# Kernel optimization log

Measured on AMD Instinct MI355X. Metric: run time of the kernel, lower is better.

## Reference

```python
import jax, jax.numpy as jnp
import numpy as np

N = 100000      # nodes
E = 1600000     # edges
IN, H1, H2, OUT = 128, 128, 64, 128  # layer_channel = [128, (128+128)//2, (128+128)//4, 128]


def setup_inputs() -> dict:
    key = jax.random.key(0)
    ks = jax.random.split(key, 11)
    w = lambda k, s: (jax.random.normal(k, s, jnp.float32) * 0.05)
    return {
        "x": jax.random.normal(ks[0], (N, IN), jnp.float32),
        "edge_index": jax.random.randint(ks[1], (2, E), 0, N),
        "gcn1_w": w(ks[2], (IN, H1)),   "gcn1_b": jnp.zeros((H1,), jnp.float32),
        "fc2_w": w(ks[3], (H1, H1)),   # nn.Linear weight [out, in]
        "gcn3_w": w(ks[4], (H1, H2)),   "gcn3_b": jnp.zeros((H2,), jnp.float32),
        "fc4_w": w(ks[5], (H2, H2)),
        "gcn5_w": w(ks[6], (H2, OUT)),  "gcn5_b": jnp.zeros((OUT,), jnp.float32),
        "fc6_w": w(ks[7], (OUT, OUT)),
    }


def _gcn_norm(edge_index):
    # PyG GCNConv default: add self-loops, symmetric normalization D^-1/2 (A+I) D^-1/2
    loop = jnp.arange(N, dtype=edge_index.dtype)
    src = jnp.concatenate([edge_index[0], loop])
    dst = jnp.concatenate([edge_index[1], loop])
    deg = jax.ops.segment_sum(jnp.ones_like(src, jnp.float32), dst, num_segments=N)
    dinv = jnp.where(deg > 0, jax.lax.rsqrt(jnp.maximum(deg, 1.0)), 0.0)
    norm = dinv[src] * dinv[dst]  # [E+N]
    return src, dst, norm


def _gcn_conv(x, W, b, src, dst, norm):
    h = x @ W                              # [N, d_out]
    msg = h[src] * norm[:, None]           # gather + scale over edges
    return jax.ops.segment_sum(msg, dst, num_segments=N) + b


def reference(x, edge_index, gcn1_w, gcn1_b, fc2_w, gcn3_w, gcn3_b, fc4_w, gcn5_w, gcn5_b, fc6_w):
    src, dst, norm = _gcn_norm(edge_index)
    relu = jax.nn.relu
    z1 = relu(_gcn_conv(x, gcn1_w, gcn1_b, src, dst, norm))
    z1 = relu(z1 + z1 @ fc2_w.T)
    z2 = relu(_gcn_conv(z1, gcn3_w, gcn3_b, src, dst, norm))
    z2 = relu(z2 + z2 @ fc4_w.T)
    z3 = relu(_gcn_conv(z2, gcn5_w, gcn5_b, src, dst, norm))
    z3 = relu(z3 + z3 @ fc6_w.T)
    return z3
```

## Files before the change

kernel.cpp:

```cpp
#include <hip/hip_runtime.h>
#include <cstdint>
#include <cstddef>

#define NN 100000
#define NE 1600000
#define NBB 391

typedef short short8 __attribute__((ext_vector_type(8)));
typedef float floatx4 __attribute__((ext_vector_type(4)));
typedef uint32_t u32x4 __attribute__((ext_vector_type(4)));
typedef unsigned short u16;
typedef uint32_t u32;


static __global__ void k_zero(int* __restrict__ gh) {
    int i = threadIdx.x;
    if (i < NBB + 1) gh[i] = 0;
}

static __global__ __launch_bounds__(1024) void k_bhist(const int* __restrict__ dst,
                                                       int* __restrict__ gh) {
    __shared__ int h[NBB + 1];
    int t = threadIdx.x;
    for (int i = t; i < NBB; i += 1024) h[i] = 0;
    __syncthreads();
    int e0 = blockIdx.x * 4096;
#pragma unroll
    for (int j = 0; j < 4; j++) {
        int e = e0 + j * 1024 + t;
        if (e < NE) atomicAdd(&h[dst[e] >> 8], 1);
    }
    __syncthreads();
    for (int i = t; i < NBB; i += 1024)
        if (h[i]) atomicAdd(&gh[i], h[i]);
}

static __global__ void k_bscan(const int* __restrict__ gh, int* __restrict__ gbase,
                               int* __restrict__ gcur) {
    __shared__ int sd[512];
    int t = threadIdx.x;
    int v = (t < NBB) ? gh[t] : 0;
    sd[t] = v;
    __syncthreads();
    for (int off = 1; off < 512; off <<= 1) {
        int x = (t >= off) ? sd[t - off] : 0;
        __syncthreads();
        sd[t] += x;
        __syncthreads();
    }
    int excl = (t > 0) ? sd[t - 1] : 0;
    if (t < NBB) {
        gbase[t] = excl;
        gcur[t] = excl;
    }
    if (t == NBB) gbase[NBB] = excl;
}

static __global__ __launch_bounds__(1024) void k_bscatter(const int* __restrict__ src,
                                                          const int* __restrict__ dst,
                                                          int* __restrict__ gcur,
                                                          int2* __restrict__ staging) {
    __shared__ int h[NBB + 1];
    __shared__ int base[NBB + 1];
    int t = threadIdx.x;
    for (int i = t; i < NBB; i += 1024) h[i] = 0;
    __syncthreads();
    int e0 = blockIdx.x * 4096;
    int b[4], l[4], sv[4], dv[4];
#pragma unroll
    for (int j = 0; j < 4; j++) {
        int e = e0 + j * 1024 + t;
        b[j] = -1;
        if (e < NE) {
            sv[j] = src[e];
            dv[j] = dst[e];
            b[j] = dv[j] >> 8;
            l[j] = atomicAdd(&h[b[j]], 1);
        }
    }
    __syncthreads();
    for (int i = t; i < NBB; i += 1024)
        if (h[i]) base[i] = atomicAdd(&gcur[i], h[i]);
    __syncthreads();
#pragma unroll
    for (int j = 0; j < 4; j++)
        if (b[j] >= 0) staging[base[b[j]] + l[j]] = make_int2(sv[j], dv[j]);
}

static __global__ __launch_bounds__(1024) void k_blocal(const int2* __restrict__ staging,
                                                        const int* __restrict__ gbase,
                                                        int* __restrict__ deg,
                                                        float* __restrict__ dinv) {
    __shared__ int cnt[256];
    int b = blockIdx.x;
    int t = threadIdx.x;
    if (t < 256) cnt[t] = 0;
    __syncthreads();
    int end = gbase[b + 1];
    for (int i = gbase[b] + t; i < end; i += 1024)
        atomicAdd(&cnt[staging[i].y & 255], 1);
    __syncthreads();
    if (t < 256) {
        int node = (b << 8) + t;
        if (node < NN) {
            int d = cnt[t] + 1;
            deg[node] = d;
            dinv[node] = rsqrtf((float)d);
        }
    }
}

static __global__ void k_scan1(const int* __restrict__ deg, int* __restrict__ row_ptr,
                               int* __restrict__ bsums) {
    __shared__ int sd[256];
    int t = threadIdx.x;
    int base = blockIdx.x * 1024;
    int v[4];
    int s = 0;
#pragma unroll
    for (int j = 0; j < 4; j++) {
        int i = base + t * 4 + j;
        int c = (i < NN) ? (deg[i] - 1) : 0;
        v[j] = s;
        s += c;
    }
    sd[t] = s;
    __syncthreads();
    for (int off = 1; off < 256; off <<= 1) {
        int x = (t >= off) ? sd[t - off] : 0;
        __syncthreads();
        sd[t] += x;
        __syncthreads();
    }
    int excl = (t > 0) ? sd[t - 1] : 0;
#pragma unroll
    for (int j = 0; j < 4; j++) {
        int i = base + t * 4 + j;
        if (i < NN) row_ptr[i] = excl + v[j];
    }
    if (t == 255) bsums[blockIdx.x] = sd[255];
}

static __global__ void k_scan2(int* __restrict__ bsums, int nb) {
    __shared__ int sd[128];
    int t = threadIdx.x;
    int v = (t < nb) ? bsums[t] : 0;
    sd[t] = v;
    __syncthreads();
    for (int off = 1; off < 128; off <<= 1) {
        int x = (t >= off) ? sd[t - off] : 0;
        __syncthreads();
        sd[t] += x;
        __syncthreads();
    }
    if (t < nb) bsums[t] = sd[t] - v;
}

static __global__ void k_scan3(int* __restrict__ row_ptr, const int* __restrict__ bsums) {
    int i = blockIdx.x * 256 + threadIdx.x;
    if (i < NN) {
        row_ptr[i] += bsums[i >> 10];
    } else if (i == NN) {
        row_ptr[NN] = NE;
    }
}

static __global__ __launch_bounds__(1024) void k_bfill(const int2* __restrict__ staging,
                                                       const int* __restrict__ gbase,
                                                       const int* __restrict__ row_ptr,
                                                       int* __restrict__ csr_src) {
    __shared__ int cnt[256];
    int b = blockIdx.x;
    int t = threadIdx.x;
    if (t < 256) cnt[t] = 0;
    __syncthreads();
    int end = gbase[b + 1];
    for (int i = gbase[b] + t; i < end; i += 1024) {
        int2 ed = staging[i];
        int r = atomicAdd(&cnt[ed.y & 255], 1);
        csr_src[row_ptr[ed.y] + r] = ed.x;
    }
}

__device__ __forceinline__ void split_bf16(float f, short& hi, short& lo) {
    union { float f; uint32_t u; } x;
    x.f = f;
    uint32_t uh = x.u + 0x7FFFu + ((x.u >> 16) & 1u);
    hi = (short)(uh >> 16);
    union { uint32_t u; float f; } hf;
    hf.u = (uh >> 16) << 16;
    float r = f - hf.f;
    union { float f; uint32_t u; } y;
    y.f = r;
    uint32_t ul = y.u + 0x7FFFu + ((y.u >> 16) & 1u);
    lo = (short)(ul >> 16);
}

__device__ __forceinline__ u16 f2bf(float f) {
    union { float f; uint32_t u; } x;
    x.f = f;
    uint32_t r = x.u + 0x7FFFu + ((x.u >> 16) & 1u);
    return (u16)(r >> 16);
}

__device__ __forceinline__ float bf2f(u16 h) {
    union { uint32_t u; float f; } x;
    x.u = ((uint32_t)h) << 16;
    return x.f;
}

__device__ __forceinline__ u32 packsplit(float f) {
    short h, l;
    split_bf16(f, h, l);
    return (u32)(u16)h | ((u32)(u16)l << 16);
}

__device__ __forceinline__ float unpacksplit(u32 u) {
    return bf2f((u16)(u & 0xFFFFu)) + bf2f((u16)(u >> 16));
}

__device__ __forceinline__ void acc2(uint32_t u, float& a0, float& a1) {
    union { uint32_t u; float f; } lo, hi;
    lo.u = u << 16;
    hi.u = u & 0xFFFF0000u;
    a0 += lo.f;
    a1 += hi.f;
}

struct WDesc {
    const float* W;
    short* fh;
    short* fl;
    int din, dout, transb, base, total;
};
struct WPrepArgs { WDesc d[6]; };

static __global__ void k_wprep(WPrepArgs args) {
    int tid = blockIdx.x * 256 + threadIdx.x;
#pragma unroll
    for (int i = 0; i < 6; i++) {
        const WDesc& D = args.d[i];
        if (tid >= D.base && tid < D.base + D.total) {
            int local = tid - D.base;
            int lane = local & 63;
            int rest = local >> 6;
            int kst = D.din >> 5;
            int ks = rest % kst;
            int ntile = rest / kst;
            int n = ntile * 16 + (lane & 15);
            int k0 = ks * 32 + (lane >> 4) * 8;
#pragma unroll
            for (int j = 0; j < 8; j++) {
                int k = k0 + j;
                float v = D.transb ? D.W[(size_t)n * D.din + k]
                                   : D.W[(size_t)k * D.dout + n];
                short h, l;
                split_bf16(v, h, l);
                D.fh[(size_t)local * 8 + j] = h;
                D.fl[(size_t)local * 8 + j] = l;
            }
        }
    }
}

template <int DIN, int DOUT, int MT, int AMODE, int OMODE, bool RESID, bool BIAS, bool SCALE>
__global__ __launch_bounds__(256) void k_mgemm(const void* __restrict__ Av,
                                               const short* __restrict__ fh,
                                               const short* __restrict__ fl,
                                               const float* __restrict__ bias,
                                               const float* __restrict__ dinv,
                                               void* __restrict__ C) {
    static_assert(!RESID || DIN == DOUT, "residual needs square");
    constexpr int KST = DIN / 32;
    constexpr int NTW = DOUT / 64;
    const int t = threadIdx.x;
    const int wave = t >> 6;
    const int lane = t & 63;
    const int r16 = lane & 15;
    const int kq = lane >> 4;

    const float* Af = (const float*)Av;
    const u32*   Au = (const u32*)Av;

    short8 bh[NTW][KST], bl[NTW][KST];
#pragma unroll
    for (int nt = 0; nt < NTW; nt++) {
        int ntile = wave * NTW + nt;
#pragma unroll
        for (int ks = 0; ks < KST; ks++) {
            size_t o = ((size_t)(ntile * KST + ks) * 64 + lane) * 8;
            bh[nt][ks] = *(const short8*)(fh + o);
            bl[nt][ks] = *(const short8*)(fl + o);
        }
    }

    const int m0b = blockIdx.x * (MT * 16);
#pragma unroll 1
    for (int mt = 0; mt < MT; mt++) {
        const int m0 = m0b + mt * 16;
        if (m0 >= NN) break;
        const int ra = min(m0 + r16, NN - 1);

        floatx4 acc[NTW];
#pragma unroll
        for (int nt = 0; nt < NTW; nt++) acc[nt] = (floatx4){0.f, 0.f, 0.f, 0.f};

        if constexpr (AMODE == 1) {
            const float* Ap = Af + (size_t)ra * DIN + kq * 8;
#pragma unroll
            for (int ks = 0; ks < KST; ks++) {
                float4 f0 = *(const float4*)(Ap + ks * 32);
                float4 f1 = *(const float4*)(Ap + ks * 32 + 4);
                float fe[8] = {f0.x, f0.y, f0.z, f0.w, f1.x, f1.y, f1.z, f1.w};
                short8 ah;
#pragma unroll
                for (int j = 0; j < 8; j++) ah[j] = (short)f2bf(fe[j]);
#pragma unroll
                for (int nt = 0; nt < NTW; nt++) {
                    acc[nt] = __builtin_amdgcn_mfma_f32_16x16x32_bf16(ah, bh[nt][ks], acc[nt], 0, 0, 0);
                    acc[nt] = __builtin_amdgcn_mfma_f32_16x16x32_bf16(ah, bl[nt][ks], acc[nt], 0, 0, 0);
                }
            }
        } else {
            const u32* Ap = Au + (size_t)ra * DIN + kq * 8;
#pragma unroll
            for (int ks = 0; ks < KST; ks++) {
                u32x4 p0 = *(const u32x4*)(Ap + ks * 32);
                u32x4 p1 = *(const u32x4*)(Ap + ks * 32 + 4);
                short8 ah, al;
#pragma unroll
                for (int j = 0; j < 4; j++) {
                    ah[j] = (short)(p0[j] & 0xFFFFu);
                    al[j] = (short)(p0[j] >> 16);
                    ah[j + 4] = (short)(p1[j] & 0xFFFFu);
                    al[j + 4] = (short)(p1[j] >> 16);
                }
#pragma unroll
                for (int nt = 0; nt < NTW; nt++) {
                    acc[nt] = __builtin_amdgcn_mfma_f32_16x16x32_bf16(ah, bh[nt][ks], acc[nt], 0, 0, 0);
                    acc[nt] = __builtin_amdgcn_mfma_f32_16x16x32_bf16(ah, bl[nt][ks], acc[nt], 0, 0, 0);
                    acc[nt] = __builtin_amdgcn_mfma_f32_16x16x32_bf16(al, bh[nt][ks], acc[nt], 0, 0, 0);
                }
            }
        }

#pragma unroll
        for (int nt = 0; nt < NTW; nt++) {
            int col = (wave * NTW + nt) * 16 + r16;
#pragma unroll
            for (int r = 0; r < 4; r++) {
                int row = m0 + kq * 4 + r;
                if (row < NN) {
                    float v = acc[nt][r];
                    if constexpr (RESID)
                        v = fmaxf(v + unpacksplit(Au[(size_t)row * DIN + col]), 0.f);
                    if constexpr (BIAS) v = fmaxf(v + bias[col], 0.f);
                    if constexpr (SCALE) v *= dinv[row];
                    if constexpr (OMODE == 0)
                        ((float*)C)[(size_t)row * DOUT + col] = v;
                    else if constexpr (OMODE == 1)
                        ((u16*)C)[(size_t)row * DOUT + col] = f2bf(v);
                    else
                        ((u32*)C)[(size_t)row * DOUT + col] = packsplit(v);
                }
            }
        }
    }
}

template <int DIN, int DMID, int DOUT, int MT, bool RESID1, bool BIAS1,
          bool SCALE2, bool RESID2, int OMODE2>
__global__ __launch_bounds__(256) void k_mfused(const u32* __restrict__ A,
                                                const short* __restrict__ f1h,
                                                const short* __restrict__ f1l,
                                                const short* __restrict__ f2h,
                                                const short* __restrict__ f2l,
                                                const float* __restrict__ bias1,
                                                const float* __restrict__ dinv,
                                                void* __restrict__ C) {
    static_assert(!RESID1 || DIN == DMID, "resid1 needs square stage1");
    static_assert(!RESID2 || DMID == DOUT, "resid2 needs square stage2");
    constexpr int KST1 = DIN / 32;
    constexpr int NTW1 = DMID / 64;
    constexpr int KST2 = DMID / 32;
    constexpr int NTW2 = DOUT / 64;
    constexpr int LDW = DMID + 4;
    __shared__ u32 lds[16][LDW];

    const int t = threadIdx.x;
    const int wave = t >> 6;
    const int lane = t & 63;
    const int r16 = lane & 15;
    const int kq = lane >> 4;

    short8 b1h[NTW1][KST1], b1l[NTW1][KST1];
#pragma unroll
    for (int nt = 0; nt < NTW1; nt++) {
        int ntile = wave * NTW1 + nt;
#pragma unroll
        for (int ks = 0; ks < KST1; ks++) {
            size_t o = ((size_t)(ntile * KST1 + ks) * 64 + lane) * 8;
            b1h[nt][ks] = *(const short8*)(f1h + o);
            b1l[nt][ks] = *(const short8*)(f1l + o);
        }
    }
    short8 b2h[NTW2][KST2], b2l[NTW2][KST2];
#pragma unroll
    for (int nt = 0; nt < NTW2; nt++) {
        int ntile = wave * NTW2 + nt;
#pragma unroll
        for (int ks = 0; ks < KST2; ks++) {
            size_t o = ((size_t)(ntile * KST2 + ks) * 64 + lane) * 8;
            b2h[nt][ks] = *(const short8*)(f2h + o);
            b2l[nt][ks] = *(const short8*)(f2l + o);
        }
    }

    const int m0b = blockIdx.x * (MT * 16);
#pragma unroll 1
    for (int mt = 0; mt < MT; mt++) {
        const int m0 = m0b + mt * 16;
        if (m0 >= NN) break;
        const int ra = min(m0 + r16, NN - 1);

        floatx4 acc1[NTW1];
#pragma unroll
        for (int nt = 0; nt < NTW1; nt++) acc1[nt] = (floatx4){0.f, 0.f, 0.f, 0.f};
        {
            const u32* Ap = A + (size_t)ra * DIN + kq * 8;
#pragma unroll
            for (int ks = 0; ks < KST1; ks++) {
                u32x4 p0 = *(const u32x4*)(Ap + ks * 32);
                u32x4 p1 = *(const u32x4*)(Ap + ks * 32 + 4);
                short8 ah, al;
#pragma unroll
                for (int j = 0; j < 4; j++) {
                    ah[j] = (short)(p0[j] & 0xFFFFu);
                    al[j] = (short)(p0[j] >> 16);
                    ah[j + 4] = (short)(p1[j] & 0xFFFFu);
                    al[j + 4] = (short)(p1[j] >> 16);
                }
#pragma unroll
                for (int nt = 0; nt < NTW1; nt++) {
                    acc1[nt] = __builtin_amdgcn_mfma_f32_16x16x32_bf16(ah, b1h[nt][ks], acc1[nt], 0, 0, 0);
                    acc1[nt] = __builtin_amdgcn_mfma_f32_16x16x32_bf16(ah, b1l[nt][ks], acc1[nt], 0, 0, 0);
                    acc1[nt] = __builtin_amdgcn_mfma_f32_16x16x32_bf16(al, b1h[nt][ks], acc1[nt], 0, 0, 0);
                }
            }
        }
#pragma unroll
        for (int nt = 0; nt < NTW1; nt++) {
            int col = (wave * NTW1 + nt) * 16 + r16;
#pragma unroll
            for (int r = 0; r < 4; r++) {
                int row = m0 + kq * 4 + r;
                float v = acc1[nt][r];
                if constexpr (RESID1) {
                    if (row < NN) v = fmaxf(v + unpacksplit(A[(size_t)row * DIN + col]), 0.f);
                }
                if constexpr (BIAS1) v = fmaxf(v + bias1[col], 0.f);
                lds[kq * 4 + r][col] = packsplit(v);
            }
        }
        __syncthreads();

        floatx4 acc2[NTW2];
#pragma unroll
        for (int nt = 0; nt < NTW2; nt++) acc2[nt] = (floatx4){0.f, 0.f, 0.f, 0.f};
#pragma unroll
        for (int ks = 0; ks < KST2; ks++) {
            const u32* lp = &lds[r16][ks * 32 + kq * 8];
            u32x4 p0 = *(const u32x4*)lp;
            u32x4 p1 = *(const u32x4*)(lp + 4);
            short8 ah, al;
#pragma unroll
            for (int j = 0; j < 4; j++) {
                ah[j] = (short)(p0[j] & 0xFFFFu);
                al[j] = (short)(p0[j] >> 16);
                ah[j + 4] = (short)(p1[j] & 0xFFFFu);
                al[j + 4] = (short)(p1[j] >> 16);
            }
#pragma unroll
            for (int nt = 0; nt < NTW2; nt++) {
                acc2[nt] = __builtin_amdgcn_mfma_f32_16x16x32_bf16(ah, b2h[nt][ks], acc2[nt], 0, 0, 0);
                acc2[nt] = __builtin_amdgcn_mfma_f32_16x16x32_bf16(ah, b2l[nt][ks], acc2[nt], 0, 0, 0);
                acc2[nt] = __builtin_amdgcn_mfma_f32_16x16x32_bf16(al, b2h[nt][ks], acc2[nt], 0, 0, 0);
            }
        }

#pragma unroll
        for (int nt = 0; nt < NTW2; nt++) {
            int col = (wave * NTW2 + nt) * 16 + r16;
#pragma unroll
            for (int r = 0; r < 4; r++) {
                int row = m0 + kq * 4 + r;
                if (row < NN) {
                    float v = acc2[nt][r];
                    if constexpr (RESID2)
                        v = fmaxf(v + unpacksplit(lds[kq * 4 + r][col]), 0.f);
                    if constexpr (SCALE2) v *= dinv[row];
                    if constexpr (OMODE2 == 0)
                        ((float*)C)[(size_t)row * DOUT + col] = v;
                    else if constexpr (OMODE2 == 1)
                        ((u16*)C)[(size_t)row * DOUT + col] = f2bf(v);
                    else
                        ((u32*)C)[(size_t)row * DOUT + col] = packsplit(v);
                }
            }
        }
        __syncthreads();
    }
}

template <int D, bool BIAS_RELU>
__global__ __launch_bounds__(256) void k_agg(const u16* __restrict__ hs,
                                             const float* __restrict__ dinv,
                                             const int* __restrict__ row_ptr,
                                             const int* __restrict__ csr_src,
                                             const float* __restrict__ bias,
                                             u32* __restrict__ out) {
    constexpr int V = D / 64;
    int node = blockIdx.x * 4 + (threadIdx.x >> 6);
    int lane = threadIdx.x & 63;
    if (node >= NN) return;
    const int off = lane * V;

    float a0 = 0.f, a1 = 0.f;
    if constexpr (V == 2) {
        uint32_t u = ((const uint32_t*)(hs + (size_t)node * D))[lane];
        acc2(u, a0, a1);
    } else {
        a0 = bf2f(hs[(size_t)node * D + lane]);
    }

    int e = row_ptr[node];
    const int end = row_ptr[node + 1];

    for (; e + 8 <= end; e += 8) {
        int s[8];
#pragma unroll
        for (int i = 0; i < 8; i++) s[i] = csr_src[e + i];
        if constexpr (V == 2) {
            uint32_t v[8];
#pragma unroll
            for (int i = 0; i < 8; i++) v[i] = ((const uint32_t*)(hs + (size_t)s[i] * D))[lane];
#pragma unroll
            for (int i = 0; i < 8; i++) acc2(v[i], a0, a1);
        } else {
            u16 v[8];
#pragma unroll
            for (int i = 0; i < 8; i++) v[i] = hs[(size_t)s[i] * D + lane];
#pragma unroll
            for (int i = 0; i < 8; i++) a0 += bf2f(v[i]);
        }
    }
    for (; e + 4 <= end; e += 4) {
        int s[4];
#pragma unroll
        for (int i = 0; i < 4; i++) s[i] = csr_src[e + i];
        if constexpr (V == 2) {
            uint32_t v[4];
#pragma unroll
            for (int i = 0; i < 4; i++) v[i] = ((const uint32_t*)(hs + (size_t)s[i] * D))[lane];
#pragma unroll
            for (int i = 0; i < 4; i++) acc2(v[i], a0, a1);
        } else {
            u16 v[4];
#pragma unroll
            for (int i = 0; i < 4; i++) v[i] = hs[(size_t)s[i] * D + lane];
#pragma unroll
            for (int i = 0; i < 4; i++) a0 += bf2f(v[i]);
        }
    }
    for (; e < end; e++) {
        int s = csr_src[e];
        if constexpr (V == 2) {
            uint32_t u = ((const uint32_t*)(hs + (size_t)s * D))[lane];
            acc2(u, a0, a1);
        } else {
            a0 += bf2f(hs[(size_t)s * D + lane]);
        }
    }

    const float di = dinv[node];
    a0 *= di;
    if constexpr (V == 2) a1 *= di;
    if constexpr (BIAS_RELU) {
        a0 = fmaxf(a0 + bias[off], 0.f);
        if constexpr (V == 2) a1 = fmaxf(a1 + bias[off + 1], 0.f);
    }
    u32* po = out + (size_t)node * D + off;
    if constexpr (V == 2) {
        uint2 w;
        w.x = packsplit(a0);
        w.y = packsplit(a1);
        *(uint2*)po = w;
    } else {
        *po = packsplit(a0);
    }
}


extern "C" void kernel_launch(void* const* d_in, const int* in_sizes, int n_in,
                              void* d_out, int out_size, void* d_ws, size_t ws_size,
                              hipStream_t stream) {
    const float* x   = (const float*)d_in[0];
    const int*   ei  = (const int*)d_in[1];
    const float* g1w = (const float*)d_in[2];
    const float* g1b = (const float*)d_in[3];
    const float* f2w = (const float*)d_in[4];
    const float* g3w = (const float*)d_in[5];
    const float* g3b = (const float*)d_in[6];
    const float* f4w = (const float*)d_in[7];
    const float* g5w = (const float*)d_in[8];
    const float* g5b = (const float*)d_in[9];
    const float* f6w = (const float*)d_in[10];
    float* out = (float*)d_out;

    const int* src = ei;
    const int* dst = ei + NE;

    char* p = (char*)d_ws;
    auto alloc = [&](size_t bytes) -> void* {
        void* r = (void*)p;
        p += (bytes + 255) & ~(size_t)255;
        return r;
    };
    int*   deg     = (int*)alloc(NN * 4);
    float* dinv    = (float*)alloc(NN * 4);
    int*   row_ptr = (int*)alloc((NN + 1) * 4);
    int*   bsums   = (int*)alloc(512);
    int*   gh      = (int*)alloc((NBB + 1) * 4);
    int*   gbase   = (int*)alloc((NBB + 1) * 4);
    int*   gcur    = (int*)alloc((NBB + 1) * 4);
    int*   csr     = (int*)alloc(NE * 4);
    short* wfh     = (short*)alloc(69632 * 2);
    short* wfl     = (short*)alloc(69632 * 2);
    char* bufA = (char*)alloc((size_t)NN * 128 * 4);
    char* bufB = (char*)alloc((size_t)NN * 128 * 4);
    int2* staging  = (int2*)bufB;

    const int gE4 = (NE + 4095) / 4096;
    const int gS  = (NN + 1023) / 1024;
    const int gN1 = (NN + 1 + 255) / 256;
    const int gA  = NN / 4;
    const int gM  = (NN + 31) / 32;

    k_zero<<<1, 512, 0, stream>>>(gh);
    k_bhist<<<gE4, 1024, 0, stream>>>(dst, gh);
    k_bscan<<<1, 512, 0, stream>>>(gh, gbase, gcur);
    k_bscatter<<<gE4, 1024, 0, stream>>>(src, dst, gcur, staging);
    k_blocal<<<NBB, 1024, 0, stream>>>(staging, gbase, deg, dinv);
    k_scan1<<<gS, 256, 0, stream>>>(deg, row_ptr, bsums);
    k_scan2<<<1, 128, 0, stream>>>(bsums, gS);
    k_scan3<<<gN1, 256, 0, stream>>>(row_ptr, bsums);
    k_bfill<<<NBB, 1024, 0, stream>>>(staging, gbase, row_ptr, csr);

    {
        WPrepArgs a;
        int  eoff[6] = {0, 16384, 32768, 40960, 45056, 53248};
        int  base[6] = {0, 2048, 4096, 5120, 5632, 6656};
        int  tot[6]  = {2048, 2048, 1024, 512, 1024, 2048};
        const float* Ws[6] = {g1w, f2w, g3w, f4w, g5w, f6w};
        int din[6]  = {128, 128, 128, 64, 64, 128};
        int dout[6] = {128, 128, 64, 64, 128, 128};
        int trb[6]  = {0, 1, 0, 1, 0, 1};
        for (int i = 0; i < 6; i++) {
            a.d[i] = WDesc{Ws[i], wfh + eoff[i], wfl + eoff[i],
                           din[i], dout[i], trb[i], base[i], tot[i]};
        }
        k_wprep<<<(8704 + 255) / 256, 256, 0, stream>>>(a);
    }

    k_mgemm<128, 128, 2, 1, 1, false, false, true><<<gM, 256, 0, stream>>>(
        x, wfh + 0, wfl + 0, nullptr, dinv, bufA);
    k_agg<128, true><<<gA, 256, 0, stream>>>((const u16*)bufA, dinv, row_ptr, csr, g1b, (u32*)bufB);
    k_mfused<128, 128, 64, 2, true, false, true, false, 1><<<gM, 256, 0, stream>>>(
        (const u32*)bufB, wfh + 16384, wfl + 16384, wfh + 32768, wfl + 32768,
        nullptr, dinv, bufA);
    k_agg<64, true><<<gA, 256, 0, stream>>>((const u16*)bufA, dinv, row_ptr, csr, g3b, (u32*)bufB);
    k_mgemm<64, 64, 2, 2, 1, true, false, true><<<gM, 256, 0, stream>>>(
        bufB, wfh + 40960, wfl + 40960, nullptr, dinv, bufA);
    k_agg<64, false><<<gA, 256, 0, stream>>>((const u16*)bufA, dinv, row_ptr, csr, nullptr, (u32*)bufB);
    k_mfused<64, 128, 128, 2, false, true, false, true, 0><<<gM, 256, 0, stream>>>(
        (const u32*)bufB, wfh + 45056, wfl + 45056, wfh + 53248, wfl + 53248,
        g5b, nullptr, out);
}
```

Before: 504.0 us.

## Store split-bf16 activations as separate hi/lo planes; half-wave edge split for D=64 aggregation

Measured after the change: 508.4 us. Within noise of the previous version (+0.9%).

```diff
diff --git a/kernel.cpp b/kernel.cpp
--- a/kernel.cpp
+++ b/kernel.cpp
@@ -8,7 +8,6 @@
 
 typedef short short8 __attribute__((ext_vector_type(8)));
 typedef float floatx4 __attribute__((ext_vector_type(4)));
-typedef uint32_t u32x4 __attribute__((ext_vector_type(4)));
 typedef unsigned short u16;
 typedef uint32_t u32;
 
@@ -207,16 +206,6 @@
     union { uint32_t u; float f; } x;
     x.u = ((uint32_t)h) << 16;
     return x.f;
-}
-
-__device__ __forceinline__ u32 packsplit(float f) {
-    short h, l;
-    split_bf16(f, h, l);
-    return (u32)(u16)h | ((u32)(u16)l << 16);
-}
-
-__device__ __forceinline__ float unpacksplit(u32 u) {
-    return bf2f((u16)(u & 0xFFFFu)) + bf2f((u16)(u >> 16));
 }
 
 __device__ __forceinline__ void acc2(uint32_t u, float& a0, float& a1) {
@@ -280,7 +269,8 @@
     const int kq = lane >> 4;
 
     const float* Af = (const float*)Av;
-    const u32*   Au = (const u32*)Av;
+    const u16*   Ah = (const u16*)Av;
+    const u16*   Al = Ah + (size_t)NN * DIN;
 
     short8 bh[NTW][KST], bl[NTW][KST];
 #pragma unroll
@@ -322,19 +312,12 @@
                 }
             }
         } else {
-            const u32* Ap = Au + (size_t)ra * DIN + kq * 8;
+            const u16* Aph = Ah + (size_t)ra * DIN + kq * 8;
+            const u16* Apl = Al + (size_t)ra * DIN + kq * 8;
 #pragma unroll
             for (int ks = 0; ks < KST; ks++) {
-                u32x4 p0 = *(const u32x4*)(Ap + ks * 32);
-                u32x4 p1 = *(const u32x4*)(Ap + ks * 32 + 4);
-                short8 ah, al;
-#pragma unroll
-                for (int j = 0; j < 4; j++) {
-                    ah[j] = (short)(p0[j] & 0xFFFFu);
-                    al[j] = (short)(p0[j] >> 16);
-                    ah[j + 4] = (short)(p1[j] & 0xFFFFu);
-                    al[j + 4] = (short)(p1[j] >> 16);
-                }
+                short8 ah = *(const short8*)(Aph + ks * 32);
+                short8 al = *(const short8*)(Apl + ks * 32);
 #pragma unroll
                 for (int nt = 0; nt < NTW; nt++) {
                     acc[nt] = __builtin_amdgcn_mfma_f32_16x16x32_bf16(ah, bh[nt][ks], acc[nt], 0, 0, 0);
@@ -352,16 +335,23 @@
                 int row = m0 + kq * 4 + r;
                 if (row < NN) {
                     float v = acc[nt][r];
-                    if constexpr (RESID)
-                        v = fmaxf(v + unpacksplit(Au[(size_t)row * DIN + col]), 0.f);
+                    if constexpr (RESID) {
+                        size_t ri = (size_t)row * DIN + col;
+                        v = fmaxf(v + bf2f(Ah[ri]) + bf2f(Al[ri]), 0.f);
+                    }
                     if constexpr (BIAS) v = fmaxf(v + bias[col], 0.f);
                     if constexpr (SCALE) v *= dinv[row];
-                    if constexpr (OMODE == 0)
-                        ((float*)C)[(size_t)row * DOUT + col] = v;
-                    else if constexpr (OMODE == 1)
-                        ((u16*)C)[(size_t)row * DOUT + col] = f2bf(v);
-                    else
-                        ((u32*)C)[(size_t)row * DOUT + col] = packsplit(v);
+                    size_t oi = (size_t)row * DOUT + col;
+                    if constexpr (OMODE == 0) {
+                        ((float*)C)[oi] = v;
+                    } else if constexpr (OMODE == 1) {
+                        ((u16*)C)[oi] = f2bf(v);
+                    } else {
+                        short h, l;
+                        split_bf16(v, h, l);
+                        ((u16*)C)[oi] = (u16)h;
+                        ((u16*)C)[(size_t)NN * DOUT + oi] = (u16)l;
+                    }
                 }
             }
         }
@@ -370,7 +360,7 @@
 
 template <int DIN, int DMID, int DOUT, int MT, bool RESID1, bool BIAS1,
           bool SCALE2, bool RESID2, int OMODE2>
-__global__ __launch_bounds__(256) void k_mfused(const u32* __restrict__ A,
+__global__ __launch_bounds__(256) void k_mfused(const u16* __restrict__ Ahp,
                                                 const short* __restrict__ f1h,
                                                 const short* __restrict__ f1l,
                                                 const short* __restrict__ f2h,
@@ -384,8 +374,11 @@
     constexpr int NTW1 = DMID / 64;
     constexpr int KST2 = DMID / 32;
     constexpr int NTW2 = DOUT / 64;
-    constexpr int LDW = DMID + 4;
-    __shared__ u32 lds[16][LDW];
+    constexpr int LDW = DMID + 8;
+    __shared__ u16 ldsh[16][LDW];
+    __shared__ u16 ldsl[16][LDW];
+
+    const u16* Alp = Ahp + (size_t)NN * DIN;
 
     const int t = threadIdx.x;
     const int wave = t >> 6;
@@ -427,19 +420,12 @@
 #pragma unroll
         for (int nt = 0; nt < NTW1; nt++) acc1[nt] = (floatx4){0.f, 0.f, 0.f, 0.f};
         {
-            const u32* Ap = A + (size_t)ra * DIN + kq * 8;
+            const u16* Aph = Ahp + (size_t)ra * DIN + kq * 8;
+            const u16* Apl = Alp + (size_t)ra * DIN + kq * 8;
 #pragma unroll
             for (int ks = 0; ks < KST1; ks++) {
-                u32x4 p0 = *(const u32x4*)(Ap + ks * 32);
-                u32x4 p1 = *(const u32x4*)(Ap + ks * 32 + 4);
-                short8 ah, al;
-#pragma unroll
-                for (int j = 0; j < 4; j++) {
-                    ah[j] = (short)(p0[j] & 0xFFFFu);
-                    al[j] = (short)(p0[j] >> 16);
-                    ah[j + 4] = (short)(p1[j] & 0xFFFFu);
-                    al[j + 4] = (short)(p1[j] >> 16);
-                }
+                short8 ah = *(const short8*)(Aph + ks * 32);
+                short8 al = *(const short8*)(Apl + ks * 32);
 #pragma unroll
                 for (int nt = 0; nt < NTW1; nt++) {
                     acc1[nt] = __builtin_amdgcn_mfma_f32_16x16x32_bf16(ah, b1h[nt][ks], acc1[nt], 0, 0, 0);
@@ -456,10 +442,16 @@
                 int row = m0 + kq * 4 + r;
                 float v = acc1[nt][r];
                 if constexpr (RESID1) {
-                    if (row < NN) v = fmaxf(v + unpacksplit(A[(size_t)row * DIN + col]), 0.f);
+                    if (row < NN) {
+                        size_t ri = (size_t)row * DIN + col;
+                        v = fmaxf(v + bf2f(Ahp[ri]) + bf2f(Alp[ri]), 0.f);
+                    }
                 }
                 if constexpr (BIAS1) v = fmaxf(v + bias1[col], 0.f);
-                lds[kq * 4 + r][col] = packsplit(v);
+                short h, l;
+                split_bf16(v, h, l);
+                ldsh[kq * 4 + r][col] = (u16)h;
+                ldsl[kq * 4 + r][col] = (u16)l;
             }
         }
         __syncthreads();
@@ -469,17 +461,8 @@
         for (int nt = 0; nt < NTW2; nt++) acc2[nt] = (floatx4){0.f, 0.f, 0.f, 0.f};
 #pragma unroll
         for (int ks = 0; ks < KST2; ks++) {
-            const u32* lp = &lds[r16][ks * 32 + kq * 8];
-            u32x4 p0 = *(const u32x4*)lp;
-            u32x4 p1 = *(const u32x4*)(lp + 4);
-            short8 ah, al;
-#pragma unroll
-            for (int j = 0; j < 4; j++) {
-                ah[j] = (short)(p0[j] & 0xFFFFu);
-                al[j] = (short)(p0[j] >> 16);
-                ah[j + 4] = (short)(p1[j] & 0xFFFFu);
-                al[j + 4] = (short)(p1[j] >> 16);
-            }
+            short8 ah = *(const short8*)&ldsh[r16][ks * 32 + kq * 8];
+            short8 al = *(const short8*)&ldsl[r16][ks * 32 + kq * 8];
 #pragma unroll
             for (int nt = 0; nt < NTW2; nt++) {
                 acc2[nt] = __builtin_amdgcn_mfma_f32_16x16x32_bf16(ah, b2h[nt][ks], acc2[nt], 0, 0, 0);
@@ -497,14 +480,19 @@
                 if (row < NN) {
                     float v = acc2[nt][r];
                     if constexpr (RESID2)
-                        v = fmaxf(v + unpacksplit(lds[kq * 4 + r][col]), 0.f);
+                        v = fmaxf(v + bf2f(ldsh[kq * 4 + r][col]) + bf2f(ldsl[kq * 4 + r][col]), 0.f);
                     if constexpr (SCALE2) v *= dinv[row];
-                    if constexpr (OMODE2 == 0)
-                        ((float*)C)[(size_t)row * DOUT + col] = v;
-                    else if constexpr (OMODE2 == 1)
-                        ((u16*)C)[(size_t)row * DOUT + col] = f2bf(v);
-                    else
-                        ((u32*)C)[(size_t)row * DOUT + col] = packsplit(v);
+                    size_t oi = (size_t)row * DOUT + col;
+                    if constexpr (OMODE2 == 0) {
+                        ((float*)C)[oi] = v;
+                    } else if constexpr (OMODE2 == 1) {
+                        ((u16*)C)[oi] = f2bf(v);
+                    } else {
+                        short h, l;
+                        split_bf16(v, h, l);
+                        ((u16*)C)[oi] = (u16)h;
+                        ((u16*)C)[(size_t)NN * DOUT + oi] = (u16)l;
+                    }
                 }
             }
         }
@@ -518,85 +506,111 @@
                                              const int* __restrict__ row_ptr,
                                              const int* __restrict__ csr_src,
                                              const float* __restrict__ bias,
-                                             u32* __restrict__ out) {
-    constexpr int V = D / 64;
+                                             u16* __restrict__ outh) {
+    u16* outl = outh + (size_t)NN * D;
     int node = blockIdx.x * 4 + (threadIdx.x >> 6);
     int lane = threadIdx.x & 63;
     if (node >= NN) return;
-    const int off = lane * V;
-
-    float a0 = 0.f, a1 = 0.f;
-    if constexpr (V == 2) {
-        uint32_t u = ((const uint32_t*)(hs + (size_t)node * D))[lane];
-        acc2(u, a0, a1);
-    } else {
-        a0 = bf2f(hs[(size_t)node * D + lane]);
-    }
-
-    int e = row_ptr[node];
-    const int end = row_ptr[node + 1];
-
-    for (; e + 8 <= end; e += 8) {
-        int s[8];
-#pragma unroll
-        for (int i = 0; i < 8; i++) s[i] = csr_src[e + i];
-        if constexpr (V == 2) {
+
+    if constexpr (D == 128) {
+        const int off = lane * 2;
+        float a0 = 0.f, a1 = 0.f;
+        {
+            uint32_t u = ((const uint32_t*)(hs + (size_t)node * D))[lane];
+            acc2(u, a0, a1);
+        }
+        int e = row_ptr[node];
+        const int end = row_ptr[node + 1];
+        for (; e + 8 <= end; e += 8) {
+            int s[8];
+#pragma unroll
+            for (int i = 0; i < 8; i++) s[i] = csr_src[e + i];
             uint32_t v[8];
 #pragma unroll
             for (int i = 0; i < 8; i++) v[i] = ((const uint32_t*)(hs + (size_t)s[i] * D))[lane];
 #pragma unroll
             for (int i = 0; i < 8; i++) acc2(v[i], a0, a1);
-        } else {
-            u16 v[8];
-#pragma unroll
-            for (int i = 0; i < 8; i++) v[i] = hs[(size_t)s[i] * D + lane];
-#pragma unroll
-            for (int i = 0; i < 8; i++) a0 += bf2f(v[i]);
-        }
-    }
-    for (; e + 4 <= end; e += 4) {
-        int s[4];
-#pragma unroll
-        for (int i = 0; i < 4; i++) s[i] = csr_src[e + i];
-        if constexpr (V == 2) {
+        }
+        for (; e + 4 <= end; e += 4) {
+            int s[4];
+#pragma unroll
+            for (int i = 0; i < 4; i++) s[i] = csr_src[e + i];
             uint32_t v[4];
 #pragma unroll
             for (int i = 0; i < 4; i++) v[i] = ((const uint32_t*)(hs + (size_t)s[i] * D))[lane];
 #pragma unroll
             for (int i = 0; i < 4; i++) acc2(v[i], a0, a1);
-        } else {
-            u16 v[4];
-#pragma unroll
-            for (int i = 0; i < 4; i++) v[i] = hs[(size_t)s[i] * D + lane];
-#pragma unroll
-            for (int i = 0; i < 4; i++) a0 += bf2f(v[i]);
-        }
-    }
-    for (; e < end; e++) {
-        int s = csr_src[e];
-        if constexpr (V == 2) {
+        }
+        for (; e < end; e++) {
+            int s = csr_src[e];
             uint32_t u = ((const uint32_t*)(hs + (size_t)s * D))[lane];
             acc2(u, a0, a1);
-        } else {
-            a0 += bf2f(hs[(size_t)s * D + lane]);
-        }
-    }
-
-    const float di = dinv[node];
-    a0 *= di;
-    if constexpr (V == 2) a1 *= di;
-    if constexpr (BIAS_RELU) {
-        a0 = fmaxf(a0 + bias[off], 0.f);
-        if constexpr (V == 2) a1 = fmaxf(a1 + bias[off + 1], 0.f);
-    }
-    u32* po = out + (size_t)node * D + off;
-    if constexpr (V == 2) {
-        uint2 w;
-        w.x = packsplit(a0);
-        w.y = packsplit(a1);
-        *(uint2*)po = w;
+        }
+        const float di = dinv[node];
+        a0 *= di;
+        a1 *= di;
+        if constexpr (BIAS_RELU) {
+            a0 = fmaxf(a0 + bias[off], 0.f);
+            a1 = fmaxf(a1 + bias[off + 1], 0.f);
+        }
+        short h0, l0, h1, l1;
+        split_bf16(a0, h0, l0);
+        split_bf16(a1, h1, l1);
+        ushort2 wh, wl;
+        wh.x = (u16)h0; wh.y = (u16)h1;
+        wl.x = (u16)l0; wl.y = (u16)l1;
+        *(ushort2*)(outh + (size_t)node * D + off) = wh;
+        *(ushort2*)(outl + (size_t)node * D + off) = wl;
     } else {
-        *po = packsplit(a0);
+        const int half = lane >> 5;
+        const int l32 = lane & 31;
+        float a0 = 0.f, a1 = 0.f;
+        if (half == 0) {
+            uint32_t u = ((const uint32_t*)(hs + (size_t)node * D))[l32];
+            acc2(u, a0, a1);
+        }
+        int e = row_ptr[node];
+        const int end = row_ptr[node + 1];
+        for (; e + 8 <= end; e += 8) {
+            int s[4];
+#pragma unroll
+            for (int i = 0; i < 4; i++) s[i] = csr_src[e + half + 2 * i];
+            uint32_t v[4];
+#pragma unroll
+            for (int i = 0; i < 4; i++) v[i] = ((const uint32_t*)(hs + (size_t)s[i] * D))[l32];
+#pragma unroll
+            for (int i = 0; i < 4; i++) acc2(v[i], a0, a1);
+        }
+        for (; e + 2 <= end; e += 2) {
+            int s = csr_src[e + half];
+            uint32_t u = ((const uint32_t*)(hs + (size_t)s * D))[l32];
+            acc2(u, a0, a1);
+        }
+        if (e < end && half == 0) {
+            int s = csr_src[e];
+            uint32_t u = ((const uint32_t*)(hs + (size_t)s * D))[l32];
+            acc2(u, a0, a1);
+        }
+        a0 += __shfl_xor(a0, 32, 64);
+        a1 += __shfl_xor(a1, 32, 64);
+        if (half == 0) {
+            const int off = l32 * 2;
+            const float di = dinv[node];
+            a0 *= di;
+            a1 *= di;
+            if constexpr (BIAS_RELU) {
+                a0 = fmaxf(a0 + bias[off], 0.f);
+                a1 = fmaxf(a1 + bias[off + 1], 0.f);
+            }
+            short h0, l0, h1, l1;
+            split_bf16(a0, h0, l0);
+            split_bf16(a1, h1, l1);
+            ushort2 wh, wl;
+            wh.x = (u16)h0; wh.y = (u16)h1;
+            wl.x = (u16)l0; wl.y = (u16)l1;
+            *(ushort2*)(outh + (size_t)node * D + off) = wh;
+            *(ushort2*)(outl + (size_t)node * D + off) = wl;
+        }
     }
 }
 
@@ -674,15 +688,15 @@
 
     k_mgemm<128, 128, 2, 1, 1, false, false, true><<<gM, 256, 0, stream>>>(
         x, wfh + 0, wfl + 0, nullptr, dinv, bufA);
-    k_agg<128, true><<<gA, 256, 0, stream>>>((const u16*)bufA, dinv, row_ptr, csr, g1b, (u32*)bufB);
+    k_agg<128, true><<<gA, 256, 0, stream>>>((const u16*)bufA, dinv, row_ptr, csr, g1b, (u16*)bufB);
     k_mfused<128, 128, 64, 2, true, false, true, false, 1><<<gM, 256, 0, stream>>>(
-        (const u32*)bufB, wfh + 16384, wfl + 16384, wfh + 32768, wfl + 32768,
+        (const u16*)bufB, wfh + 16384, wfl + 16384, wfh + 32768, wfl + 32768,
         nullptr, dinv, bufA);
-    k_agg<64, true><<<gA, 256, 0, stream>>>((const u16*)bufA, dinv, row_ptr, csr, g3b, (u32*)bufB);
+    k_agg<64, true><<<gA, 256, 0, stream>>>((const u16*)bufA, dinv, row_ptr, csr, g3b, (u16*)bufB);
     k_mgemm<64, 64, 2, 2, 1, true, false, true><<<gM, 256, 0, stream>>>(
         bufB, wfh + 40960, wfl + 40960, nullptr, dinv, bufA);
-    k_agg<64, false><<<gA, 256, 0, stream>>>((const u16*)bufA, dinv, row_ptr, csr, nullptr, (u32*)bufB);
+    k_agg<64, false><<<gA, 256, 0, stream>>>((const u16*)bufA, dinv, row_ptr, csr, nullptr, (u16*)bufB);
     k_mfused<64, 128, 128, 2, false, true, false, true, 0><<<gM, 256, 0, stream>>>(
-        (const u32*)bufB, wfh + 45056, wfl + 45056, wfh + 53248, wfl + 53248,
+        (const u16*)bufB, wfh + 45056, wfl + 45056, wfh + 53248, wfl + 53248,
         g5b, nullptr, out);
 }
```
